# Performance work log

Measured on AMD Instinct MI355X. Metric: run time of the kernel, lower is better.

## Reference

```python
import jax, jax.numpy as jnp
import numpy as np

N_NODES = 50000
N_EDGES = 800000
D_MODEL = 256
NUM_HEADS = 8
HEAD_DIM = D_MODEL // NUM_HEADS
D_FF = 2 * D_MODEL
NEG_SLOPE = 0.2
BN_EPS = 1e-5


def setup_inputs() -> dict:
    key = jax.random.key(0)
    ks = jax.random.split(key, 16)
    x = jax.random.normal(ks[0], (N_NODES, D_MODEL), dtype=jnp.float32)
    # edges guaranteed self-loop-free (remove_self_loops is then a no-op)
    src = jax.random.randint(ks[1], (N_EDGES,), 0, N_NODES)
    off = jax.random.randint(ks[2], (N_EDGES,), 1, N_NODES)
    dst = (src + off) % N_NODES
    edge_index = jnp.stack([src, dst]).astype(jnp.int64)

    def lin(k, fi, fo):
        s = 1.0 / np.sqrt(fi)
        return jax.random.uniform(k, (fi, fo), jnp.float32, -s, s)

    inp = {
        'x': x, 'edge_index': edge_index,
        'Wq': lin(ks[3], D_MODEL, D_MODEL), 'bq': jnp.zeros((D_MODEL,), jnp.float32),
        'Wk': lin(ks[4], D_MODEL, D_MODEL), 'bk': jnp.zeros((D_MODEL,), jnp.float32),
        'Wv': lin(ks[5], D_MODEL, D_MODEL), 'bv': jnp.zeros((D_MODEL,), jnp.float32),
        'Wo': lin(ks[6], D_MODEL, D_MODEL), 'bo': jnp.zeros((D_MODEL,), jnp.float32),
        'W1': lin(ks[7], D_MODEL, D_FF), 'b1': jnp.zeros((D_FF,), jnp.float32),
        'W2': lin(ks[8], D_FF, D_MODEL), 'b2': jnp.zeros((D_MODEL,), jnp.float32),
        'bn1_g': jnp.ones((D_MODEL,), jnp.float32), 'bn1_b': jnp.zeros((D_MODEL,), jnp.float32),
        'bn2_g': jnp.ones((D_MODEL,), jnp.float32), 'bn2_b': jnp.zeros((D_MODEL,), jnp.float32),
    }
    return inp


def _batch_norm(h, g, b):
    mean = jnp.mean(h, axis=0)
    var = jnp.mean((h - mean) ** 2, axis=0)  # biased var, torch BN training mode
    return (h - mean) * jax.lax.rsqrt(var + BN_EPS) * g + b


def reference(x, edge_index, Wq, bq, Wk, bk, Wv, bv, Wo, bo, W1, b1, W2, b2,
              bn1_g, bn1_b, bn2_g, bn2_b):
    N = x.shape[0]
    Qh = (x @ Wq + bq).reshape(N, NUM_HEADS, HEAD_DIM)
    Kh = (x @ Wk + bk).reshape(N, NUM_HEADS, HEAD_DIM)
    Vh = (x @ Wv + bv).reshape(N, NUM_HEADS, HEAD_DIM)
    # per-node score q_n . k_n / sqrt(C)  -> [N, H]
    s = jnp.einsum('nhc,nhc->nh', Qh, Kh) / jnp.sqrt(jnp.float32(HEAD_DIM))

    # add self loops (input edges contain no self loops)
    loops = jnp.arange(N, dtype=edge_index.dtype)
    src = jnp.concatenate([edge_index[0], loops])
    dst = jnp.concatenate([edge_index[1], loops])

    alpha = jax.nn.leaky_relu(s[src] + s[dst], NEG_SLOPE)  # [Etot, H]
    # segment softmax over destination neighborhoods
    m = jax.ops.segment_max(alpha, dst, num_segments=N)
    e = jnp.exp(alpha - m[dst])
    denom = jax.ops.segment_sum(e, dst, num_segments=N)
    a = e / denom[dst]

    msg = Vh[src] * a[:, :, None]                     # [Etot, H, C]
    attn = jax.ops.segment_sum(msg, dst, num_segments=N).reshape(N, D_MODEL)

    h = attn @ Wo + bo
    h = x + h
    h = _batch_norm(h, bn1_g, bn1_b)
    h2 = jax.nn.relu(h @ W1 + b1) @ W2 + b2
    h = _batch_norm(h + h2, bn2_g, bn2_b)
    return h
```

## Files before the change

### kernel.cpp

```cpp
#include <hip/hip_runtime.h>
#include <hip/hip_bf16.h>

#define NN 50000
#define MP 50048
#define DM 256
#define NH 8
#define HD 32
#define DFF 512

typedef unsigned short u16;
typedef unsigned char u8;
typedef __attribute__((ext_vector_type(8))) short bf16x8;
typedef __attribute__((ext_vector_type(4))) short bf16x4;
typedef __attribute__((ext_vector_type(4))) float f32x4;

__device__ __forceinline__ float leaky(float a) { return a > 0.f ? a : 0.2f * a; }

__device__ __forceinline__ float b2f(u16 s) {
    union { float f; unsigned u; } v; v.u = ((unsigned)s) << 16; return v.f;
}
__device__ __forceinline__ u16 f2b(float f) {
    union { float f; unsigned u; } v; v.f = f;
    unsigned r = v.u + 0x7FFFu + ((v.u >> 16) & 1u);
    return (u16)(r >> 16);
}

__device__ __forceinline__ void f8enc8(const float* v, unsigned* w2) {
#if __has_builtin(__builtin_amdgcn_cvt_pk_fp8_f32)
    int lo = 0, hi = 0;
    lo = __builtin_amdgcn_cvt_pk_fp8_f32(v[0], v[1], lo, false);
    lo = __builtin_amdgcn_cvt_pk_fp8_f32(v[2], v[3], lo, true);
    hi = __builtin_amdgcn_cvt_pk_fp8_f32(v[4], v[5], hi, false);
    hi = __builtin_amdgcn_cvt_pk_fp8_f32(v[6], v[7], hi, true);
    w2[0] = (unsigned)lo; w2[1] = (unsigned)hi;
#else
    unsigned r[8];
#pragma unroll
    for (int j = 0; j < 8; ++j) {
        union { float f; unsigned u; } x; x.f = v[j];
        const unsigned s = (x.u >> 24) & 0x80u;
        float a = fabsf(v[j]);
        if (a > 448.f) a = 448.f;
        if (a < 0.0009765625f) { r[j] = s; continue; }
        if (a < 0.015625f) {
            int m = (int)(a * 512.f + 0.5f); if (m > 7) m = 7;
            r[j] = s | (unsigned)m; continue;
        }
        union { float f; unsigned u; } w; w.f = a;
        unsigned rr = w.u + 0x7FFFFu + ((w.u >> 20) & 1u);
        int e2 = (int)((rr >> 23) & 0xffu) - 127;
        unsigned m3 = (rr >> 20) & 7u;
        if (e2 > 8) { e2 = 8; m3 = 7u; }
        r[j] = s | ((unsigned)(e2 + 7) << 3) | m3;
    }
    w2[0] = r[0] | (r[1] << 8) | (r[2] << 16) | (r[3] << 24);
    w2[1] = r[4] | (r[5] << 8) | (r[6] << 16) | (r[7] << 24);
#endif
}

__device__ __forceinline__ void f8dec8(uint2 uv, float* f) {
#if __has_builtin(__builtin_amdgcn_cvt_pk_f32_fp8)
    auto p0 = __builtin_amdgcn_cvt_pk_f32_fp8((int)uv.x, false);
    auto p1 = __builtin_amdgcn_cvt_pk_f32_fp8((int)uv.x, true);
    auto p2 = __builtin_amdgcn_cvt_pk_f32_fp8((int)uv.y, false);
    auto p3 = __builtin_amdgcn_cvt_pk_f32_fp8((int)uv.y, true);
    f[0] = p0[0]; f[1] = p0[1]; f[2] = p1[0]; f[3] = p1[1];
    f[4] = p2[0]; f[5] = p2[1]; f[6] = p3[0]; f[7] = p3[1];
#else
#pragma unroll
    for (int j = 0; j < 8; ++j) {
        const unsigned b = (j < 4 ? uv.x >> (8 * j) : uv.y >> (8 * (j - 4))) & 0xffu;
        const unsigned s = (b & 0x80u) << 24;
        const unsigned em = b & 0x7fu;
        union { unsigned u; float f; } n; n.u = s | ((em + 0x3C0u) << 20);
        float dn = (float)(int)(em & 7u) * 0.001953125f;
        dn = (b & 0x80u) ? -dn : dn;
        f[j] = (em >= 8u) ? n.f : dn;
    }
#endif
}

#define ASYNC16(gp, lp) __builtin_amdgcn_global_load_lds( \
    (const __attribute__((address_space(1))) void*)(gp),  \
    (__attribute__((address_space(3))) void*)(lp), 16, 0, 0)

template<int RELU, int RES, int K, int MODE>
__global__ __launch_bounds__(256, 4) void gemm_bf16(
    const u16* __restrict__ A, const u16* __restrict__ Bt,
    const float* __restrict__ bias, const void* __restrict__ res,
    const float* __restrict__ ra, const float* __restrict__ rb,
    u16* __restrict__ C, u8* __restrict__ Cv, float* __restrict__ gsums,
    int M, int N)
{
    union SMu {
        struct { u16 As[128][64]; u16 Bs[128][64]; } t;
        struct { u16 eps[128][136]; float lsum[128], lsq[128]; } e;
    };
    __shared__ __align__(16) SMu sm;

    const int tid = threadIdx.x;
    const int wave = tid >> 6, lane = tid & 63;

    const int gx = gridDim.x;
    const int nwg = gx * gridDim.y;
    const int orig = blockIdx.y * gx + blockIdx.x;
    const int q = nwg >> 3, r = nwg & 7;
    const int xcd = orig & 7, rank = orig >> 3;
    const int wg = (xcd < r ? xcd * (q + 1) : r * (q + 1) + (xcd - r) * q) + rank;
    const int m0 = (wg / gx) * 128, n0 = (wg % gx) * 128;

    const int wr = (wave >> 1) * 64, wc = (wave & 1) * 64;

    f32x4 acc[4][4] = {};

    const int srow = wave * 32 + (lane >> 3);
    const int scol = ((lane & 7) * 8) ^ (((lane >> 3) & 7) << 3);
    const int rx = (lane & 7) << 4;

#pragma unroll
    for (int k0 = 0; k0 < K; k0 += 64) {
#pragma unroll
        for (int i = 0; i < 4; ++i)
            ASYNC16(A + (size_t)(m0 + srow + i * 8) * K + k0 + scol,
                    &sm.t.As[wave * 32 + i * 8][0]);
#pragma unroll
        for (int i = 0; i < 4; ++i)
            ASYNC16(Bt + (size_t)(n0 + srow + i * 8) * K + k0 + scol,
                    &sm.t.Bs[wave * 32 + i * 8][0]);
        __syncthreads();
        const char* asb = (const char*)&sm.t.As[0][0];
        const char* bsb = (const char*)&sm.t.Bs[0][0];
#pragma unroll
        for (int kk = 0; kk < 64; kk += 32) {
            const int kb = (kk + (lane >> 4) * 8) * 2;
            bf16x8 av[4], bv[4];
#pragma unroll
            for (int m = 0; m < 4; ++m) {
                const int rr_ = wr + m * 16 + (lane & 15);
                av[m] = *(const bf16x8*)(asb + rr_ * 128 + (kb ^ rx));
            }
#pragma unroll
            for (int n = 0; n < 4; ++n) {
                const int rr_ = wc + n * 16 + (lane & 15);
                bv[n] = *(const bf16x8*)(bsb + rr_ * 128 + (kb ^ rx));
            }
#pragma unroll
            for (int m = 0; m < 4; ++m)
#pragma unroll
                for (int n = 0; n < 4; ++n)
                    acc[m][n] = __builtin_amdgcn_mfma_f32_16x16x32_bf16(
                        av[m], bv[n], acc[m][n], 0, 0, 0);
        }
        __syncthreads();
    }

    const int col_l = lane & 15, rgrp = (lane >> 4) * 4;
#pragma unroll
    for (int m = 0; m < 4; ++m)
#pragma unroll
        for (int rr2 = 0; rr2 < 4; ++rr2) {
            const int lr = wr + m * 16 + rgrp + rr2;
#pragma unroll
            for (int n = 0; n < 4; ++n)
                sm.e.eps[lr][wc + n * 16 + col_l] = f2b(acc[m][n][rr2]);
        }
    __syncthreads();
    if (MODE == 2) {
        if (tid < 128) { sm.e.lsum[tid] = 0.f; sm.e.lsq[tid] = 0.f; }
        __syncthreads();
    }

    const int tc = (tid & 15) * 8;
    float bb[8];
    *(float4*)(bb)     = *(const float4*)(bias + n0 + tc);
    *(float4*)(bb + 4) = *(const float4*)(bias + n0 + tc + 4);
    float ra8[8], rb8[8];
    if (RES == 3) {
        *(float4*)(ra8)     = *(const float4*)(ra + n0 + tc);
        *(float4*)(ra8 + 4) = *(const float4*)(ra + n0 + tc + 4);
        *(float4*)(rb8)     = *(const float4*)(rb + n0 + tc);
        *(float4*)(rb8 + 4) = *(const float4*)(rb + n0 + tc + 4);
    }
    float psum[8] = {}, psq[8] = {};
    const bool v8 = (MODE == 1) && (n0 >= 512);
    u16* dstb = (MODE == 1) ? C + n0 : C + n0;
    size_t dstride = (MODE == 1) ? 512 : (size_t)N;
    u8* vdst = v8 ? (Cv + (n0 - 512)) : nullptr;

#pragma unroll
    for (int it = 0; it < 8; ++it) {
        const int tr = (tid >> 4) + it * 16;
        const int row = m0 + tr;
        if (row < M) {
            bf16x8 cv = *(const bf16x8*)((const char*)&sm.e.eps[0][0] + tr * 272 + tc * 2);
            float v[8];
#pragma unroll
            for (int j = 0; j < 8; ++j) v[j] = b2f((u16)cv[j]) + bb[j];
            if (RES == 1) {
                const float* rp = (const float*)res + (size_t)row * N + n0 + tc;
                float4 r0 = *(const float4*)(rp);
                float4 r1 = *(const float4*)(rp + 4);
                v[0] += r0.x; v[1] += r0.y; v[2] += r0.z; v[3] += r0.w;
                v[4] += r1.x; v[5] += r1.y; v[6] += r1.z; v[7] += r1.w;
            }
            if (RES == 2) {
                bf16x8 rv = *(const bf16x8*)((const u16*)res + (size_t)row * N + n0 + tc);
#pragma unroll
                for (int j = 0; j < 8; ++j) v[j] += b2f((u16)rv[j]);
            }
            if (RES == 3) {
                bf16x8 rv = *(const bf16x8*)((const u16*)res + (size_t)row * N + n0 + tc);
#pragma unroll
                for (int j = 0; j < 8; ++j) v[j] += b2f((u16)rv[j]) * ra8[j] + rb8[j];
            }
            if (RELU) {
#pragma unroll
                for (int j = 0; j < 8; ++j) v[j] = fmaxf(v[j], 0.f);
            }
            if (MODE == 2) {
#pragma unroll
                for (int j = 0; j < 8; ++j) { psum[j] += v[j]; psq[j] += v[j] * v[j]; }
            }
            if (v8) {
                unsigned w2[2];
                f8enc8(v, w2);
                *(uint2*)(vdst + (size_t)row * 256 + tc) = make_uint2(w2[0], w2[1]);
            } else {
                u16 o[8];
#pragma unroll
                for (int j = 0; j < 8; ++j) o[j] = f2b(v[j]);
                *(bf16x8*)(dstb + (size_t)row * dstride + tc) = *(bf16x8*)o;
            }
        }
    }

    if (MODE == 2) {
#pragma unroll
        for (int j = 0; j < 8; ++j) {
            atomicAdd(&sm.e.lsum[tc + j], psum[j]);
            atomicAdd(&sm.e.lsq[tc + j], psq[j]);
        }
        __syncthreads();
        if (tid < 128) {
            atomicAdd(&gsums[n0 + tid], sm.e.lsum[tid]);
            atomicAdd(&gsums[DM + n0 + tid], sm.e.lsq[tid]);
        }
    }
}

__global__ __launch_bounds__(256) void prep_kernel(
    const float* __restrict__ x, u16* __restrict__ xb,
    const float* __restrict__ Wq, const float* __restrict__ Wk,
    const float* __restrict__ Wv, const float* __restrict__ Wo,
    const float* __restrict__ W1, const float* __restrict__ W2,
    u16* __restrict__ wqkvt, u16* __restrict__ wot,
    u16* __restrict__ w1t, u16* __restrict__ w2t,
    const float* __restrict__ bq, const float* __restrict__ bk,
    const float* __restrict__ bv, float* __restrict__ bqkv,
    const int* __restrict__ edst, int* __restrict__ counts, int E)
{
    const int b = blockIdx.x;
    if (b < 6250) {
        const size_t i = ((size_t)b * 256 + threadIdx.x) * 8;
        float4 a = *(const float4*)(x + i);
        float4 c = *(const float4*)(x + i + 4);
        u16 o[8] = {f2b(a.x), f2b(a.y), f2b(a.z), f2b(a.w),
                    f2b(c.x), f2b(c.y), f2b(c.z), f2b(c.w)};
        *(bf16x8*)(xb + i) = *(bf16x8*)o;
    } else if (b < 6378) {
        __shared__ float tile[64][65];
        const int tb = b - 6250;
        const float* Wsrc; u16* outp; int srcN, outS, n0, k0;
        if (tb < 64) {
            const int mi = tb >> 4, ti = tb & 15;
            n0 = (ti & 3) * 64; k0 = (ti >> 2) * 64;
            srcN = 256; outS = 256;
            if (mi == 0)      { Wsrc = Wq; outp = wqkvt; }
            else if (mi == 1) { Wsrc = Wk; outp = wqkvt + 256 * 256; }
            else if (mi == 2) { Wsrc = Wv; outp = wqkvt + 512 * 256; }
            else              { Wsrc = Wo; outp = wot; }
        } else if (tb < 96) {
            const int ti = tb - 64;
            n0 = (ti & 7) * 64; k0 = (ti >> 3) * 64;
            srcN = 512; outS = 256; Wsrc = W1; outp = w1t;
        } else {
            const int ti = tb - 96;
            n0 = (ti & 3) * 64; k0 = (ti >> 2) * 64;
            srcN = 256; outS = 512; Wsrc = W2; outp = w2t;
        }
        const int kr = threadIdx.x >> 4, cc = (threadIdx.x & 15) * 4;
#pragma unroll
        for (int j = 0; j < 4; ++j) {
            float4 v = *(const float4*)(Wsrc + (size_t)(k0 + kr + j * 16) * srcN + n0 + cc);
            tile[kr + j * 16][cc + 0] = v.x;
            tile[kr + j * 16][cc + 1] = v.y;
            tile[kr + j * 16][cc + 2] = v.z;
            tile[kr + j * 16][cc + 3] = v.w;
        }
        __syncthreads();
        const int nr = threadIdx.x >> 3, c2 = (threadIdx.x & 7) * 8;
#pragma unroll
        for (int p = 0; p < 2; ++p) {
            const int row = nr + p * 32;
            u16 o[8];
#pragma unroll
            for (int j = 0; j < 8; ++j) o[j] = f2b(tile[c2 + j][row]);
            *(bf16x8*)(outp + (size_t)(n0 + row) * outS + k0 + c2) = *(bf16x8*)o;
        }
    } else if (b == 6378) {
        const int t = threadIdx.x;
        bqkv[t] = bq[t]; bqkv[t + 256] = bk[t]; bqkv[t + 512] = bv[t];
    } else {
        const int e = (b - 6379) * 256 + threadIdx.x;
        if (e < E) atomicAdd(&counts[edst[e]], 1);
    }
}

__global__ __launch_bounds__(256) void bnfold_kernel(
    const float* __restrict__ sums, const float* __restrict__ g,
    const float* __restrict__ be, u16* __restrict__ w1t,
    const float* __restrict__ W1, const float* __restrict__ b1,
    float* __restrict__ b1p, float* __restrict__ affa, float* __restrict__ affc)
{
    const int blk = blockIdx.x;
    const int k = threadIdx.x;
    const float invM = 1.f / (float)NN;
    const float mean = sums[k] * invM;
    const float var = sums[DM + k] * invM - mean * mean;
    const float a = g[k] * rsqrtf(var + 1e-5f);
    const float c = be[k] - mean * a;
    if (blk < 64) {
#pragma unroll
        for (int j = 0; j < 8; ++j) {
            u16* pp = w1t + (size_t)(blk * 8 + j) * 256 + k;
            *pp = f2b(b2f(*pp) * a);
        }
    } else {
        __shared__ float cs[256];
        cs[k] = c;
        if (blk == 64) { affa[k] = a; affc[k] = c; }
        __syncthreads();
        const int n = (blk - 64) * 256 + k;
        float acc = b1[n];
        for (int kk = 0; kk < 256; ++kk)
            acc += cs[kk] * W1[(size_t)kk * 512 + n];
        b1p[n] = acc;
    }
}

__global__ __launch_bounds__(256) void scorefill_kernel(
    const u16* __restrict__ QK, float* __restrict__ s,
    const int* __restrict__ esrc, const int* __restrict__ edst,
    int* __restrict__ cursor, int* __restrict__ csr, int E, int nsb)
{
    const int b = blockIdx.x;
    if (b < nsb) {
        const int t = b * 256 + threadIdx.x;
        if (t >= NN * NH) return;
        const int n = t >> 3, h = t & 7;
        const u16* qp = QK + (size_t)n * 512 + h * HD;
        const u16* kp = qp + DM;
        float acc = 0.f;
#pragma unroll
        for (int c = 0; c < HD; c += 8) {
            bf16x8 qa = *(const bf16x8*)(qp + c);
            bf16x8 ka = *(const bf16x8*)(kp + c);
#pragma unroll
            for (int j = 0; j < 8; ++j)
                acc += b2f((u16)qa[j]) * b2f((u16)ka[j]);
        }
        s[t] = acc * 0.17677669529663687f;
    } else {
        const int e = (b - nsb) * 256 + threadIdx.x;
        if (e >= E) return;
        const int p = atomicAdd(&cursor[edst[e]], 1);
        csr[p] = esrc[e];
    }
}

__global__ __launch_bounds__(1024) void scan_kernel(
    const int* __restrict__ counts, int* __restrict__ offs,
    int* __restrict__ cursor, int n)
{
    __shared__ int wsum[16];
    __shared__ int srun;
    const int tid = threadIdx.x, lane = tid & 63, wid = tid >> 6;
    if (tid == 0) srun = 0;
    for (int base = 0; base < n; base += 4096) {
        const int idx = base + tid * 4;
        int v0 = 0, v1 = 0, v2 = 0, v3 = 0;
        if (idx + 3 < n) {
            int4 qv = *(const int4*)(counts + idx);
            v0 = qv.x; v1 = qv.y; v2 = qv.z; v3 = qv.w;
        } else if (idx < n) {
            v0 = counts[idx];
            if (idx + 1 < n) v1 = counts[idx + 1];
            if (idx + 2 < n) v2 = counts[idx + 2];
        }
        const int tsum = v0 + v1 + v2 + v3;
        int sc = tsum;
#pragma unroll
        for (int off = 1; off < 64; off <<= 1) {
            int t = __shfl_up(sc, off);
            if (lane >= off) sc += t;
        }
        if (lane == 63) wsum[wid] = sc;
        __syncthreads();
        if (tid < 16) {
            int w = wsum[tid];
#pragma unroll
            for (int off = 1; off < 16; off <<= 1) {
                int t = __shfl_up(w, off);
                if (tid >= off) w += t;
            }
            wsum[tid] = w;
        }
        __syncthreads();
        const int run = srun;
        int e = run + (wid ? wsum[wid - 1] : 0) + sc - tsum;
        if (idx < n)     { offs[idx] = e;     cursor[idx] = e; }
        e += v0;
        if (idx + 1 < n) { offs[idx + 1] = e; cursor[idx + 1] = e; }
        e += v1;
        if (idx + 2 < n) { offs[idx + 2] = e; cursor[idx + 2] = e; }
        e += v2;
        if (idx + 3 < n) { offs[idx + 3] = e; cursor[idx + 3] = e; }
        const int tot = wsum[15];
        __syncthreads();
        if (tid == 0) srun = run + tot;
    }
    if (tid == 0) offs[n] = srun;
}

__global__ __launch_bounds__(256) void aggregate_kernel(
    const float* __restrict__ s, const u8* __restrict__ V,
    const int* __restrict__ offs, const int* __restrict__ srcs,
    u16* __restrict__ attn)
{
    const int n = (blockIdx.x * 256 + threadIdx.x) >> 6;
    const int lane = threadIdx.x & 63;
    if (n >= NN) return;
    const int base = offs[n];
    const int deg = offs[n + 1] - base;
    const int half = lane >> 5;
    const int l = lane & 31;
    const int f0 = l * 8;
    const int h0 = l >> 2;
    const float snh = s[(size_t)n * 8 + h0];

    float a[8] = {};
    float d = 0.f;
    if (half == 0) {
        const float w = __expf(fminf(leaky(2.f * snh), 30.f));
        d = w;
        float vf[8];
        f8dec8(*(const uint2*)(V + (size_t)n * 256 + f0), vf);
#pragma unroll
        for (int j = 0; j < 8; ++j) a[j] = w * vf[j];
    }

    int i = 0;
    for (; i + 8 <= deg; i += 8) {
        const int sr0 = srcs[base + i + 0 + half];
        const int sr1 = srcs[base + i + 2 + half];
        const int sr2 = srcs[base + i + 4 + half];
        const int sr3 = srcs[base + i + 6 + half];
        const float sv0 = s[(size_t)sr0 * 8 + h0];
        const float sv1 = s[(size_t)sr1 * 8 + h0];
        const float sv2 = s[(size_t)sr2 * 8 + h0];
        const float sv3 = s[(size_t)sr3 * 8 + h0];
        uint2 q0 = *(const uint2*)(V + (size_t)sr0 * 256 + f0);
        uint2 q1 = *(const uint2*)(V + (size_t)sr1 * 256 + f0);
        uint2 q2 = *(const uint2*)(V + (size_t)sr2 * 256 + f0);
        uint2 q3 = *(const uint2*)(V + (size_t)sr3 * 256 + f0);
        const float w0 = __expf(fminf(leaky(snh + sv0), 30.f));
        const float w1 = __expf(fminf(leaky(snh + sv1), 30.f));
        const float w2 = __expf(fminf(leaky(snh + sv2), 30.f));
        const float w3 = __expf(fminf(leaky(snh + sv3), 30.f));
        d += w0 + w1 + w2 + w3;
        float u0[8], u1[8], u2[8], u3[8];
        f8dec8(q0, u0); f8dec8(q1, u1); f8dec8(q2, u2); f8dec8(q3, u3);
#pragma unroll
        for (int j = 0; j < 8; ++j)
            a[j] += w0 * u0[j] + w1 * u1[j] + w2 * u2[j] + w3 * u3[j];
    }
    for (; i + 2 <= deg; i += 2) {
        const int sr = srcs[base + i + half];
        const float sv = s[(size_t)sr * 8 + h0];
        uint2 qv = *(const uint2*)(V + (size_t)sr * 256 + f0);
        const float w = __expf(fminf(leaky(snh + sv), 30.f));
        float uf[8];
        f8dec8(qv, uf);
        d += w;
#pragma unroll
        for (int j = 0; j < 8; ++j) a[j] += w * uf[j];
    }
    if (i < deg && half == 0) {
        const int sr = srcs[base + i];
        const float sv = s[(size_t)sr * 8 + h0];
        uint2 qv = *(const uint2*)(V + (size_t)sr * 256 + f0);
        const float w = __expf(fminf(leaky(snh + sv), 30.f));
        float uf[8];
        f8dec8(qv, uf);
        d += w;
#pragma unroll
        for (int j = 0; j < 8; ++j) a[j] += w * uf[j];
    }

    d += __shfl_xor(d, 32);
#pragma unroll
    for (int j = 0; j < 8; ++j) a[j] += __shfl_xor(a[j], 32);

    if (half == 0) {
        const float rd = 1.f / d;
        u16 o[8];
#pragma unroll
        for (int j = 0; j < 8; ++j) o[j] = f2b(a[j] * rd);
        *(bf16x8*)(attn + (size_t)n * DM + f0) = *(bf16x8*)o;
    }
}

__global__ __launch_bounds__(256) void apply_out_kernel(
    const u16* __restrict__ z, const float* __restrict__ sums,
    const float* __restrict__ g, const float* __restrict__ b,
    float* __restrict__ out)
{
    const size_t i = ((size_t)blockIdx.x * 256 + threadIdx.x) * 8;
    if (i >= (size_t)NN * DM) return;
    const int f0 = (int)(i & (DM - 1));
    const float invM = 1.f / (float)NN;
    bf16x8 v = *(const bf16x8*)(z + i);
    float o[8];
#pragma unroll
    for (int j = 0; j < 8; ++j) {
        const int f = f0 + j;
        const float mean = sums[f] * invM;
        const float var = sums[DM + f] * invM - mean * mean;
        const float a = g[f] * rsqrtf(var + 1e-5f);
        o[j] = b2f((u16)v[j]) * a + (b[f] - mean * a);
    }
    *(float4*)(out + i)     = *(float4*)(o);
    *(float4*)(out + i + 4) = *(float4*)(o + 4);
}

extern "C" void kernel_launch(void* const* d_in, const int* in_sizes, int n_in,
                              void* d_out, int out_size, void* d_ws, size_t ws_size,
                              hipStream_t stream)
{
    const float* x   = (const float*)d_in[0];
    const int* eidx  = (const int*)d_in[1];
    const int E      = in_sizes[1] / 2;
    const int* esrc  = eidx;
    const int* edst  = eidx + E;
    const float* Wq = (const float*)d_in[2];  const float* bq = (const float*)d_in[3];
    const float* Wk = (const float*)d_in[4];  const float* bk = (const float*)d_in[5];
    const float* Wv = (const float*)d_in[6];  const float* bv = (const float*)d_in[7];
    const float* Wo = (const float*)d_in[8];  const float* bo = (const float*)d_in[9];
    const float* W1 = (const float*)d_in[10]; const float* b1 = (const float*)d_in[11];
    const float* W2 = (const float*)d_in[12]; const float* b2 = (const float*)d_in[13];
    const float* g1 = (const float*)d_in[14]; const float* be1 = (const float*)d_in[15];
    const float* g2 = (const float*)d_in[16]; const float* be2 = (const float*)d_in[17];
    float* out = (float*)d_out;

    u16* xb  = (u16*)d_ws;
    u16* qk  = xb + (size_t)MP * DM;
    u8*  vb  = (u8*)(qk + (size_t)MP * 512);
    u16* attn = (u16*)(vb) + (size_t)MP * DM;
    float* sS = (float*)(attn + (size_t)MP * DM);
    int* counts = (int*)(sS + (size_t)NN * NH);
    int* offs   = counts + NN;
    int* cursor = offs + NN + 1;
    int* csr    = cursor + NN;
    uintptr_t p = (uintptr_t)(csr + E);
    p = (p + 15) & ~(uintptr_t)15;
    u16* wqkvt = (u16*)p;
    u16* wot   = wqkvt + 768 * 256;
    u16* w1t   = wot + 256 * 256;
    u16* w2t   = w1t + 512 * 256;
    float* bqkv   = (float*)(w2t + 256 * 512);
    float* bnsum1 = bqkv + 768;
    float* bnsum2 = bnsum1 + 512;
    float* b1p    = bnsum2 + 512;
    float* affa   = b1p + 512;
    float* affc   = affa + 256;

    const dim3 blk(256);
    const int elem_grid = (NN * DM / 8 + 255) / 256;
    const int hist_blks = (E + 255) / 256;
    const int nsb = (NN * NH + 255) / 256;

    hipMemsetAsync(counts, 0, sizeof(int) * NN, stream);
    hipMemsetAsync(bnsum1, 0, sizeof(float) * 1024, stream);
    prep_kernel<<<6379 + hist_blks, blk, 0, stream>>>(
        x, xb, Wq, Wk, Wv, Wo, W1, W2, wqkvt, wot, w1t, w2t,
        bq, bk, bv, bqkv, edst, counts, E);
    scan_kernel<<<1, 1024, 0, stream>>>(counts, offs, cursor, NN);

    gemm_bf16<0, 0, 256, 1><<<dim3(6, MP / 128), blk, 0, stream>>>(
        xb, wqkvt, bqkv, nullptr, nullptr, nullptr, qk, vb, nullptr, NN, 768);

    scorefill_kernel<<<nsb + hist_blks, blk, 0, stream>>>(
        qk, sS, esrc, edst, cursor, csr, E, nsb);

    aggregate_kernel<<<(NN + 3) / 4, blk, 0, stream>>>(sS, vb, offs, csr, attn);

    gemm_bf16<0, 2, 256, 2><<<dim3(2, MP / 128), blk, 0, stream>>>(
        attn, wot, bo, xb, nullptr, nullptr, xb, nullptr, bnsum1, NN, DM);

    bnfold_kernel<<<66, blk, 0, stream>>>(bnsum1, g1, be1, w1t, W1, b1,
                                          b1p, affa, affc);

    gemm_bf16<1, 0, 256, 0><<<dim3(4, MP / 128), blk, 0, stream>>>(
        xb, w1t, b1p, nullptr, nullptr, nullptr, qk, nullptr, nullptr, NN, DFF);

    gemm_bf16<0, 3, 512, 2><<<dim3(2, MP / 128), blk, 0, stream>>>(
        qk, w2t, b2, xb, affa, affc, attn, nullptr, bnsum2, NN, DM);

    apply_out_kernel<<<elem_grid, blk, 0, stream>>>(attn, bnsum2, g2, be2, out);
}
```

Measured before the change: 358.7 us.

## Fuse CSR fill into QKV GEMM grid and vectorize edge atomics

Extra blocks are appended to the QKV GEMM grid so that the CSR scatter fill runs concurrently with the matmul, and the score computation becomes its own kernel. The edge histogram and fill loops now handle four edges per thread using int4 loads. The intent is to hide the atomic-heavy CSR build behind GEMM compute and to cut per-edge index load overhead. The trade-off is that fill blocks compete with GEMM tiles for CUs, and the XCD remap now uses the fixed MROWS constant.

Result: no change. 362.8 us (+1.1%).

```diff
diff --git a/kernel.cpp b/kernel.cpp
--- a/kernel.cpp
+++ b/kernel.cpp
@@ -3,6 +3,7 @@
 
 #define NN 50000
 #define MP 50048
+#define MROWS 391
 #define DM 256
 #define NH 8
 #define HD 32
@@ -84,14 +85,36 @@
     (const __attribute__((address_space(1))) void*)(gp),  \
     (__attribute__((address_space(3))) void*)(lp), 16, 0, 0)
 
-template<int RELU, int RES, int K, int MODE>
+template<int RELU, int RES, int K, int MODE, int FILL>
 __global__ __launch_bounds__(256, 4) void gemm_bf16(
     const u16* __restrict__ A, const u16* __restrict__ Bt,
     const float* __restrict__ bias, const void* __restrict__ res,
     const float* __restrict__ ra, const float* __restrict__ rb,
     u16* __restrict__ C, u8* __restrict__ Cv, float* __restrict__ gsums,
+    const int* __restrict__ esrc, const int* __restrict__ edst,
+    int* __restrict__ cursor, int* __restrict__ csr, int E,
     int M, int N)
 {
+    if (FILL && blockIdx.y >= MROWS) {
+        const int fb = (blockIdx.y - MROWS) * gridDim.x + blockIdx.x;
+        const int e0 = (fb * 256 + (int)threadIdx.x) * 4;
+        if (e0 + 3 < E) {
+            const int4 s4 = *(const int4*)(esrc + e0);
+            const int4 d4 = *(const int4*)(edst + e0);
+            const int p0 = atomicAdd(&cursor[d4.x], 1);
+            const int p1 = atomicAdd(&cursor[d4.y], 1);
+            const int p2 = atomicAdd(&cursor[d4.z], 1);
+            const int p3 = atomicAdd(&cursor[d4.w], 1);
+            csr[p0] = s4.x; csr[p1] = s4.y; csr[p2] = s4.z; csr[p3] = s4.w;
+        } else {
+            for (int e = e0; e < E; ++e) {
+                const int p = atomicAdd(&cursor[edst[e]], 1);
+                csr[p] = esrc[e];
+            }
+        }
+        return;
+    }
+
     union SMu {
         struct { u16 As[128][64]; u16 Bs[128][64]; } t;
         struct { u16 eps[128][136]; float lsum[128], lsq[128]; } e;
@@ -102,7 +125,7 @@
     const int wave = tid >> 6, lane = tid & 63;
 
     const int gx = gridDim.x;
-    const int nwg = gx * gridDim.y;
+    const int nwg = gx * MROWS;
     const int orig = blockIdx.y * gx + blockIdx.x;
     const int q = nwg >> 3, r = nwg & 7;
     const int xcd = orig & 7, rank = orig >> 3;
@@ -183,7 +206,7 @@
     }
     float psum[8] = {}, psq[8] = {};
     const bool v8 = (MODE == 1) && (n0 >= 512);
-    u16* dstb = (MODE == 1) ? C + n0 : C + n0;
+    u16* dstb = C + n0;
     size_t dstride = (MODE == 1) ? 512 : (size_t)N;
     u8* vdst = v8 ? (Cv + (n0 - 512)) : nullptr;
 
@@ -311,8 +334,16 @@
         const int t = threadIdx.x;
         bqkv[t] = bq[t]; bqkv[t + 256] = bk[t]; bqkv[t + 512] = bv[t];
     } else {
-        const int e = (b - 6379) * 256 + threadIdx.x;
-        if (e < E) atomicAdd(&counts[edst[e]], 1);
+        const int e0 = ((b - 6379) * 256 + (int)threadIdx.x) * 4;
+        if (e0 + 3 < E) {
+            const int4 d4 = *(const int4*)(edst + e0);
+            atomicAdd(&counts[d4.x], 1);
+            atomicAdd(&counts[d4.y], 1);
+            atomicAdd(&counts[d4.z], 1);
+            atomicAdd(&counts[d4.w], 1);
+        } else {
+            for (int e = e0; e < E; ++e) atomicAdd(&counts[edst[e]], 1);
+        }
     }
 }
 
@@ -348,34 +379,24 @@
     }
 }
 
-__global__ __launch_bounds__(256) void scorefill_kernel(
-    const u16* __restrict__ QK, float* __restrict__ s,
-    const int* __restrict__ esrc, const int* __restrict__ edst,
-    int* __restrict__ cursor, int* __restrict__ csr, int E, int nsb)
-{
-    const int b = blockIdx.x;
-    if (b < nsb) {
-        const int t = b * 256 + threadIdx.x;
-        if (t >= NN * NH) return;
-        const int n = t >> 3, h = t & 7;
-        const u16* qp = QK + (size_t)n * 512 + h * HD;
-        const u16* kp = qp + DM;
-        float acc = 0.f;
-#pragma unroll
-        for (int c = 0; c < HD; c += 8) {
-            bf16x8 qa = *(const bf16x8*)(qp + c);
-            bf16x8 ka = *(const bf16x8*)(kp + c);
-#pragma unroll
-            for (int j = 0; j < 8; ++j)
-                acc += b2f((u16)qa[j]) * b2f((u16)ka[j]);
-        }
-        s[t] = acc * 0.17677669529663687f;
-    } else {
-        const int e = (b - nsb) * 256 + threadIdx.x;
-        if (e >= E) return;
-        const int p = atomicAdd(&cursor[edst[e]], 1);
-        csr[p] = esrc[e];
-    }
+__global__ __launch_bounds__(256) void score_kernel(
+    const u16* __restrict__ QK, float* __restrict__ s)
+{
+    const int t = blockIdx.x * 256 + threadIdx.x;
+    if (t >= NN * NH) return;
+    const int n = t >> 3, h = t & 7;
+    const u16* qp = QK + (size_t)n * 512 + h * HD;
+    const u16* kp = qp + DM;
+    float acc = 0.f;
+#pragma unroll
+    for (int c = 0; c < HD; c += 8) {
+        bf16x8 qa = *(const bf16x8*)(qp + c);
+        bf16x8 ka = *(const bf16x8*)(kp + c);
+#pragma unroll
+        for (int j = 0; j < 8; ++j)
+            acc += b2f((u16)qa[j]) * b2f((u16)ka[j]);
+    }
+    s[t] = acc * 0.17677669529663687f;
 }
 
 __global__ __launch_bounds__(1024) void scan_kernel(
@@ -586,8 +607,8 @@
 
     const dim3 blk(256);
     const int elem_grid = (NN * DM / 8 + 255) / 256;
-    const int hist_blks = (E + 255) / 256;
-    const int nsb = (NN * NH + 255) / 256;
+    const int hist_blks = (E / 4 + 255) / 256;
+    const int fill_rows = (hist_blks + 5) / 6;
 
     hipMemsetAsync(counts, 0, sizeof(int) * NN, stream);
     hipMemsetAsync(bnsum1, 0, sizeof(float) * 1024, stream);
@@ -596,25 +617,28 @@
         bq, bk, bv, bqkv, edst, counts, E);
     scan_kernel<<<1, 1024, 0, stream>>>(counts, offs, cursor, NN);
 
-    gemm_bf16<0, 0, 256, 1><<<dim3(6, MP / 128), blk, 0, stream>>>(
-        xb, wqkvt, bqkv, nullptr, nullptr, nullptr, qk, vb, nullptr, NN, 768);
-
-    scorefill_kernel<<<nsb + hist_blks, blk, 0, stream>>>(
-        qk, sS, esrc, edst, cursor, csr, E, nsb);
+    gemm_bf16<0, 0, 256, 1, 1><<<dim3(6, MROWS + fill_rows), blk, 0, stream>>>(
+        xb, wqkvt, bqkv, nullptr, nullptr, nullptr, qk, vb, nullptr,
+        esrc, edst, cursor, csr, E, NN, 768);
+
+    score_kernel<<<(NN * NH + 255) / 256, blk, 0, stream>>>(qk, sS);
 
     aggregate_kernel<<<(NN + 3) / 4, blk, 0, stream>>>(sS, vb, offs, csr, attn);
 
-    gemm_bf16<0, 2, 256, 2><<<dim3(2, MP / 128), blk, 0, stream>>>(
-        attn, wot, bo, xb, nullptr, nullptr, xb, nullptr, bnsum1, NN, DM);
+    gemm_bf16<0, 2, 256, 2, 0><<<dim3(2, MROWS), blk, 0, stream>>>(
+        attn, wot, bo, xb, nullptr, nullptr, xb, nullptr, bnsum1,
+        nullptr, nullptr, nullptr, nullptr, 0, NN, DM);
 
     bnfold_kernel<<<66, blk, 0, stream>>>(bnsum1, g1, be1, w1t, W1, b1,
                                           b1p, affa, affc);
 
-    gemm_bf16<1, 0, 256, 0><<<dim3(4, MP / 128), blk, 0, stream>>>(
-        xb, w1t, b1p, nullptr, nullptr, nullptr, qk, nullptr, nullptr, NN, DFF);
-
-    gemm_bf16<0, 3, 512, 2><<<dim3(2, MP / 128), blk, 0, stream>>>(
-        qk, w2t, b2, xb, affa, affc, attn, nullptr, bnsum2, NN, DM);
+    gemm_bf16<1, 0, 256, 0, 0><<<dim3(4, MROWS), blk, 0, stream>>>(
+        xb, w1t, b1p, nullptr, nullptr, nullptr, qk, nullptr, nullptr,
+        nullptr, nullptr, nullptr, nullptr, 0, NN, DFF);
+
+    gemm_bf16<0, 3, 512, 2, 0><<<dim3(2, MROWS), blk, 0, stream>>>(
+        qk, w2t, b2, xb, affa, affc, attn, nullptr, bnsum2,
+        nullptr, nullptr, nullptr, nullptr, 0, NN, DM);
 
     apply_out_kernel<<<elem_grid, blk, 0, stream>>>(attn, bnsum2, g2, be2, out);
 }
```
